# Kernel tuning notes

Hardware: AMD Instinct MI355X
Metric: run time of the kernel (lower is better)

Reference implementation:

```python
import jax, jax.numpy as jnp
import numpy as np

N_TAXA = 32   # N taxa
K = 256       # particles
T = 16        # live subtrees at this step (t = N - r)
R = 16        # merges already done
S = 1024      # alignment sites
A = 4         # DNA alphabet
D = 64        # embedding dim
C = 16        # site-position feature dim
PRIOR_LEN = 0.1


def _expm4(M):
    """Matrix exponential of [..., A, A] via scaling-and-squaring + Taylor."""
    n_sq = 6
    Ms = M / (2.0 ** n_sq)
    I = jnp.eye(M.shape[-1], dtype=M.dtype)
    P = I + Ms
    Tm = Ms
    for i in range(2, 7):
        Tm = jnp.matmul(Tm, Ms) / i
        P = P + Tm
    for _ in range(n_sq):
        P = jnp.matmul(P, P)
    return P


def _stat_probs(emb_ExD, site_SxC, W_stat, W_site):
    # q_matrix_decoder.stat_probs_VxSxA: per-node, per-site stationary probs
    logits = emb_ExD @ W_stat                     # [E, A]
    logits = logits[:, None, :] + site_SxC @ W_site  # [E, S, A]
    return jax.nn.softmax(logits, axis=-1)


def setup_inputs() -> dict:
    key = jax.random.key(0)
    ks = jax.random.split(key, 10)
    ldf = np.zeros(2 * N_TAXA, np.float32)
    for n in range(2, 2 * N_TAXA):
        ldf[n] = ldf[n - 2] + np.log(n)
    return {
        "log_weight_K": jax.random.normal(ks[0], (K,), jnp.float32),
        "branch1_lengths_Kxr": jax.random.uniform(ks[1], (K, R), jnp.float32) * 0.2 + 1e-3,
        "branch2_lengths_Kxr": jax.random.uniform(ks[2], (K, R), jnp.float32) * 0.2 + 1e-3,
        "leaf_counts_Kxt": jnp.ones((K, T), jnp.int32),
        "embeddings_KxtxD": jax.random.normal(ks[3], (K, T, D), jnp.float32),
        "log_felsensteins_KxtxSxA": jax.nn.log_softmax(
            jax.random.normal(ks[4], (K, T, S, A), jnp.float32), axis=-1),
        "log_pi_K": jax.random.normal(ks[5], (K,), jnp.float32),
        "site_positions_SxC": jax.random.uniform(ks[6], (S, C), jnp.float32),
        "W_stat": jax.random.normal(ks[7], (D, A), jnp.float32) * 0.1,
        "W_site": jax.random.normal(ks[8], (C, A), jnp.float32) * 0.1,
        "log_double_factorials_2N": jnp.asarray(ldf),
    }


def reference(log_weight_K, branch1_lengths_Kxr, branch2_lengths_Kxr,
              leaf_counts_Kxt, embeddings_KxtxD, log_felsensteins_KxtxSxA,
              log_pi_K, site_positions_SxC, W_stat, W_site,
              log_double_factorials_2N):
    K_, T_, S_, A_ = log_felsensteins_KxtxSxA.shape
    key = jax.random.key(42)
    kres, ki, koff, ku1, ku2 = jax.random.split(key, 5)

    # ---- SMC categorical resampling over particles ----
    idxK = jax.random.categorical(kres, log_weight_K, shape=(K_,))
    b1r = branch1_lengths_Kxr[idxK]
    b2r = branch2_lengths_Kxr[idxK]
    lc = leaf_counts_Kxt[idxK]
    emb = embeddings_KxtxD[idxK]
    logf = log_felsensteins_KxtxSxA[idxK]
    prev_log_pi = log_pi_K[idxK]

    # ---- proposal (J=1): uniform pair + exponential branch lengths ----
    i = jax.random.randint(ki, (K_,), 0, T_)
    off = jax.random.randint(koff, (K_,), 1, T_)
    j = (i + off) % T_
    idx1 = jnp.minimum(i, j)
    idx2 = jnp.maximum(i, j)
    branch1 = -PRIOR_LEN * jnp.log(jax.random.uniform(ku1, (K_,), minval=1e-6, maxval=1.0))
    branch2 = -PRIOR_LEN * jnp.log(jax.random.uniform(ku2, (K_,), minval=1e-6, maxval=1.0))
    ar = jnp.arange(K_)
    new_emb = 0.5 * (emb[ar, idx1] + emb[ar, idx2])  # [K, D]
    log_v_plus = jnp.log(T_ * (T_ - 1) / 2.0)        # log #pairs

    # ---- merge: put merged value at idx1, move last slot into idx2, drop last ----
    def merge(arr, new_val):
        arr = arr.at[ar, idx1].set(new_val)
        arr = arr.at[ar, idx2].set(arr[ar, T_ - 1])
        return arr[:, :T_ - 1]

    lc_new = merge(lc, lc[ar, idx1] + lc[ar, idx2])   # [K, t-1]
    emb_new = merge(emb, new_emb)                     # [K, t-1, D]

    # ---- Felsenstein pruning step for the merged node ----
    stat = _stat_probs(new_emb, site_positions_SxC, W_stat, W_site)  # [K,S,A]
    Q = jnp.broadcast_to(stat[:, :, None, :], (K_, S_, A_, A_)) - jnp.eye(A_, dtype=stat.dtype)
    P1 = _expm4(Q * branch1[:, None, None, None])  # [K,S,A,A]
    P2 = _expm4(Q * branch2[:, None, None, None])
    f1 = jnp.exp(logf[ar, idx1])  # [K,S,A]
    f2 = jnp.exp(logf[ar, idx2])
    new_logf = (jnp.log(jnp.einsum('ksab,ksb->ksa', P1, f1) + 1e-30)
                + jnp.log(jnp.einsum('ksab,ksb->ksa', P2, f2) + 1e-30))
    logf_new = merge(logf, new_logf)  # [K, t-1, S, A]

    # ---- log pi over the forest: per-subtree likelihood + priors ----
    t_new = T_ - 1
    stat_all = _stat_probs(emb_new.reshape(K_ * t_new, -1), site_positions_SxC,
                           W_stat, W_site).reshape(K_, t_new, S_, A_)
    log_stat = jnp.log(stat_all)
    L = jnp.sum(jax.scipy.special.logsumexp(logf_new + log_stat, axis=-1), axis=-1)  # [K,t-1]
    topo_idx = jnp.clip(2 * lc_new - 3, 0, 2 * N_TAXA - 1)
    topo = -log_double_factorials_2N[topo_idx] * (lc_new >= 2).astype(L.dtype)
    b1_all = jnp.concatenate([b1r, branch1[:, None]], axis=1)  # [K, r+1]
    b2_all = jnp.concatenate([b2r, branch2[:, None]], axis=1)
    prior = (jnp.sum(-b1_all / PRIOR_LEN, axis=1) + jnp.sum(-b2_all / PRIOR_LEN, axis=1)
             - 2.0 * (b1_all.shape[1]) * jnp.log(jnp.asarray(PRIOR_LEN, L.dtype)))
    log_pi_new = jnp.sum(L + topo, axis=1) + prior

    # ---- importance weight ----
    log_v_minus = jnp.log(jnp.maximum(jnp.sum((lc_new > 1).astype(L.dtype), axis=1), 1.0))
    log_weight_new = log_pi_new - prev_log_pi + log_v_minus - log_v_plus
    return log_weight_new
```

## Files before the change

kernel.cpp:

```cpp
#include <hip/hip_runtime.h>
#include <stdint.h>


#define TF_ROT(x0,x1,r) { x0 += x1; x1 = ((x1<<(r))|(x1>>(32-(r)))); x1 ^= x0; }

__host__ __device__ inline void tf2x32(uint32_t k0, uint32_t k1,
                                       uint32_t x0, uint32_t x1,
                                       uint32_t& o0, uint32_t& o1) {
  uint32_t ks2 = k0 ^ k1 ^ 0x1BD11BDAu;
  x0 += k0; x1 += k1;
  TF_ROT(x0,x1,13) TF_ROT(x0,x1,15) TF_ROT(x0,x1,26) TF_ROT(x0,x1,6)
  x0 += k1; x1 += ks2 + 1u;
  TF_ROT(x0,x1,17) TF_ROT(x0,x1,29) TF_ROT(x0,x1,16) TF_ROT(x0,x1,24)
  x0 += ks2; x1 += k0 + 2u;
  TF_ROT(x0,x1,13) TF_ROT(x0,x1,15) TF_ROT(x0,x1,26) TF_ROT(x0,x1,6)
  x0 += k0; x1 += k1 + 3u;
  TF_ROT(x0,x1,17) TF_ROT(x0,x1,29) TF_ROT(x0,x1,16) TF_ROT(x0,x1,24)
  x0 += k1; x1 += ks2 + 4u;
  TF_ROT(x0,x1,13) TF_ROT(x0,x1,15) TF_ROT(x0,x1,26) TF_ROT(x0,x1,6)
  x0 += ks2; x1 += k0 + 5u;
  o0 = x0; o1 = x1;
}

struct Keys {
  uint32_t kres0, kres1;
  uint32_t k2i0, k2i1;
  uint32_t k1o0, k1o1;
  uint32_t k2o0, k2o1;
  uint32_t ku10, ku11;
  uint32_t ku20, ku21;
};

__device__ inline uint32_t rb_fold(uint32_t k0, uint32_t k1, uint32_t i) {
  uint32_t o0, o1;
  tf2x32(k0, k1, 0u, i, o0, o1);
  return o0 ^ o1;
}

__device__ inline float u01f(uint32_t b) {
  return __uint_as_float((b >> 9) | 0x3F800000u) - 1.0f;
}

#define TINYF 1.17549435e-38f

__global__ __launch_bounds__(1024) void k_all(
    const float* __restrict__ logw, const float* __restrict__ b1r,
    const float* __restrict__ b2r, const int* __restrict__ lc,
    const float* __restrict__ emb, const float* __restrict__ lfg,
    const float* __restrict__ logpi, const float* __restrict__ site,
    const float* __restrict__ Wstat, const float* __restrict__ Wsite,
    const float* __restrict__ ldf, float* __restrict__ out, Keys kk) {
  int k = blockIdx.x, tid = threadIdx.x;
  __shared__ float sval[256];
  __shared__ int   sidx[256];
  __shared__ float enl[64];
  __shared__ float sredt[256];
  __shared__ float sredm[16];
  __shared__ float sh_m[4];
  __shared__ float sh_w1, sh_w2, sh_cw;
  __shared__ int   sh_i1, sh_i2;

  if (tid < 256) {
    uint32_t b = rb_fold(kk.kres0, kk.kres1, (uint32_t)(k * 256 + tid));
    float u = fmaxf(TINYF, u01f(b) + TINYF);
    float g = -logf(-logf(u));
    sval[tid] = g + logw[tid];
    sidx[tid] = tid;
  }
  __syncthreads();
  for (int st = 128; st > 0; st >>= 1) {
    if (tid < st) {
      float va = sval[tid], vb = sval[tid + st];
      int ia = sidx[tid], ib = sidx[tid + st];
      if (vb > va || (vb == va && ib < ia)) { sval[tid] = vb; sidx[tid] = ib; }
    }
    __syncthreads();
  }
  int p = sidx[0];

  float es0, es1, es2, es3;
  {
    int s = tid;
    float a0 = 0.f, a1 = 0.f, a2 = 0.f, a3 = 0.f;
#pragma unroll
    for (int c = 0; c < 16; c++) {
      float sc = site[s * 16 + c];
      a0 += sc * Wsite[c * 4 + 0];
      a1 += sc * Wsite[c * 4 + 1];
      a2 += sc * Wsite[c * 4 + 2];
      a3 += sc * Wsite[c * 4 + 3];
    }
    es0 = __expf(a0); es1 = __expf(a1); es2 = __expf(a2); es3 = __expf(a3);
  }

  if (tid >= 64 && tid < 128) {
    int q = tid - 64;
    int t = q >> 2, a = q & 3;
    const float4* e4 = (const float4*)(emb + ((size_t)p * 16 + t) * 64);
    float acc = 0.0f;
#pragma unroll
    for (int d4 = 0; d4 < 16; d4++) {
      float4 e = e4[d4];
      acc += e.x * Wstat[(d4 * 4 + 0) * 4 + a] + e.y * Wstat[(d4 * 4 + 1) * 4 + a] +
             e.z * Wstat[(d4 * 4 + 2) * 4 + a] + e.w * Wstat[(d4 * 4 + 3) * 4 + a];
    }
    enl[q] = __expf(acc);
  }

  if (tid < 5) {
    uint32_t i = rb_fold(kk.k2i0, kk.k2i1, (uint32_t)k) & 15u;
    uint32_t h = rb_fold(kk.k1o0, kk.k1o1, (uint32_t)k) % 15u;
    uint32_t l = rb_fold(kk.k2o0, kk.k2o1, (uint32_t)k) % 15u;
    uint32_t off = 1u + (h + l) % 15u;
    uint32_t j = (i + off) & 15u;
    int i1 = (int)(i < j ? i : j);
    int i2 = (int)(i < j ? j : i);

    if (tid < 4) {
      if (tid == 0) { sh_i1 = i1; sh_i2 = i2; }
      int a = tid;
      const float* e1p = emb + ((size_t)p * 16 + i1) * 64;
      const float* e2p = emb + ((size_t)p * 16 + i2) * 64;
      float acc = 0.0f;
      for (int d = 0; d < 64; d++) acc += 0.5f * (e1p[d] + e2p[d]) * Wstat[d * 4 + a];
      sh_m[a] = __expf(acc);
    } else {
      const float SUBR = 1.0f - 1e-6f;
      float u1 = fmaxf(1e-6f, u01f(rb_fold(kk.ku10, kk.ku11, (uint32_t)k)) * SUBR + 1e-6f);
      float u2 = fmaxf(1e-6f, u01f(rb_fold(kk.ku20, kk.ku21, (uint32_t)k)) * SUBR + 1e-6f);
      float b1 = -0.1f * logf(u1);
      float b2 = -0.1f * logf(u2);
      sh_w1 = 1.0f - expf(-b1);
      sh_w2 = 1.0f - expf(-b2);

      float sb = b1 + b2;
      for (int r = 0; r < 16; r++) sb += b1r[p * 16 + r] + b2r[p * 16 + r];
      float prior = -sb / 0.1f - 34.0f * logf(0.1f);

      float topo_sum = 0.0f; int cnt = 0;
      for (int t = 0; t < 15; t++) {
        int lct;
        if (t == i1)      lct = lc[p * 16 + i1] + lc[p * 16 + i2];
        else if (t == i2) lct = lc[p * 16 + 15];
        else              lct = lc[p * 16 + t];
        int ti = 2 * lct - 3; ti = ti < 0 ? 0 : (ti > 63 ? 63 : ti);
        if (lct >= 2) topo_sum -= ldf[ti];
        if (lct > 1) cnt++;
      }
      float log_v_minus = logf(fmaxf((float)cnt, 1.0f));
      float log_v_plus = logf(120.0f);
      sh_cw = prior + topo_sum - logpi[p] + log_v_minus - log_v_plus;
    }
  }
  __syncthreads();

  const float* base = lfg + (size_t)p * 65536;
  int s = tid;
  float acc[16];
#pragma unroll
  for (int t = 0; t < 16; t++) {
    float4 lf = *(const float4*)(base + t * 4096 + s * 4);
    float w0 = enl[t * 4 + 0] * es0, w1 = enl[t * 4 + 1] * es1;
    float w2 = enl[t * 4 + 2] * es2, w3 = enl[t * 4 + 3] * es3;
    float S1 = w0 + w1 + w2 + w3;
    float S2 = __expf(lf.x) * w0 + __expf(lf.y) * w1 +
               __expf(lf.z) * w2 + __expf(lf.w) * w3;
    acc[t] = __log2f(S2) - __log2f(S1);
  }
#pragma unroll
  for (int t = 0; t < 16; t++) {
    float v = acc[t];
    for (int o = 32; o > 0; o >>= 1) v += __shfl_down(v, o, 64);
    if ((tid & 63) == 0) sredt[t * 16 + (tid >> 6)] = v;
  }

  {
    int i1 = sh_i1, i2 = sh_i2;
    float w1 = sh_w1, w2 = sh_w2;
    float om1 = 1.0f - w1, om2 = 1.0f - w2;
    float m0 = sh_m[0], m1 = sh_m[1], m2 = sh_m[2], m3 = sh_m[3];
    float t0 = m0 * es0, t1 = m1 * es1, t2 = m2 * es2, t3 = m3 * es3;
    float T = t0 + t1 + t2 + t3;
    float invT = 1.0f / T;
    float4 lf1 = *(const float4*)(base + i1 * 4096 + s * 4);
    float4 lf2 = *(const float4*)(base + i2 * 4096 + s * 4);
    float f10 = __expf(lf1.x), f11 = __expf(lf1.y), f12 = __expf(lf1.z), f13 = __expf(lf1.w);
    float f20 = __expf(lf2.x), f21 = __expf(lf2.y), f22 = __expf(lf2.z), f23 = __expf(lf2.w);
    float dot1 = (t0 * f10 + t1 * f11 + t2 * f12 + t3 * f13) * invT;
    float dot2 = (t0 * f20 + t1 * f21 + t2 * f22 + t3 * f23) * invT;
    float n0 = __logf(om1 * f10 + w1 * dot1 + 1e-30f) + __logf(om2 * f20 + w2 * dot2 + 1e-30f);
    float n1 = __logf(om1 * f11 + w1 * dot1 + 1e-30f) + __logf(om2 * f21 + w2 * dot2 + 1e-30f);
    float n2 = __logf(om1 * f12 + w1 * dot1 + 1e-30f) + __logf(om2 * f22 + w2 * dot2 + 1e-30f);
    float n3 = __logf(om1 * f13 + w1 * dot1 + 1e-30f) + __logf(om2 * f23 + w2 * dot2 + 1e-30f);
    float S2 = __expf(n0) * t0 + __expf(n1) * t1 + __expf(n2) * t2 + __expf(n3) * t3;
    float tot = __logf(S2) - __logf(T);

    for (int o = 32; o > 0; o >>= 1) tot += __shfl_down(tot, o, 64);
    if ((tid & 63) == 0) sredm[tid >> 6] = tot;
  }
  __syncthreads();

  if (tid < 64) {
    int t = tid & 15, sb = tid >> 4;
    int i1 = sh_i1, i2 = sh_i2;
    float s4 = sredt[t * 16 + sb * 4 + 0] + sredt[t * 16 + sb * 4 + 1] +
               sredt[t * 16 + sb * 4 + 2] + sredt[t * 16 + sb * 4 + 3];
    float Lv = s4 * 0.69314718056f;
    float coef = (t == i1 || t == i2) ? 0.0f : 1.0f;
    float v = coef * Lv;
    if (tid < 16) v += sredm[tid];
    for (int o = 32; o > 0; o >>= 1) v += __shfl_down(v, o, 64);
    if (tid == 0) out[k] = sh_cw + v;
  }
}

extern "C" void kernel_launch(void* const* d_in, const int* in_sizes, int n_in,
                              void* d_out, int out_size, void* d_ws, size_t ws_size,
                              hipStream_t stream) {
  const float* logw  = (const float*)d_in[0];
  const float* b1r   = (const float*)d_in[1];
  const float* b2r   = (const float*)d_in[2];
  const int*   lc    = (const int*)d_in[3];
  const float* emb   = (const float*)d_in[4];
  const float* lfg   = (const float*)d_in[5];
  const float* logpi = (const float*)d_in[6];
  const float* site  = (const float*)d_in[7];
  const float* Wstat = (const float*)d_in[8];
  const float* Wsite = (const float*)d_in[9];
  const float* ldf   = (const float*)d_in[10];

  uint32_t S0[5], S1[5];
  for (uint32_t i = 0; i < 5; i++) tf2x32(0u, 42u, 0u, i, S0[i], S1[i]);
  Keys kk;
  kk.kres0 = S0[0]; kk.kres1 = S1[0];
  kk.ku10  = S0[3]; kk.ku11  = S1[3];
  kk.ku20  = S0[4]; kk.ku21  = S1[4];
  {
    uint32_t a0, a1, b0, b1;
    tf2x32(S0[1], S1[1], 0u, 0u, a0, a1);
    tf2x32(S0[1], S1[1], 0u, 1u, b0, b1);
    (void)a0; (void)a1;
    kk.k2i0 = b0; kk.k2i1 = b1;
  }
  {
    uint32_t a0, a1, b0, b1;
    tf2x32(S0[2], S1[2], 0u, 0u, a0, a1);
    tf2x32(S0[2], S1[2], 0u, 1u, b0, b1);
    kk.k1o0 = a0; kk.k1o1 = a1;
    kk.k2o0 = b0; kk.k2o1 = b1;
  }

  k_all<<<256, 1024, 0, stream>>>(logw, b1r, b2r, lc, emb, lfg, logpi,
                                  site, Wstat, Wsite, ldf, (float*)d_out, kk);
}
```

Measured before the change: 131.3 us.

## Use wave-shuffle argmax and issue felsenstein loads before the setup sync

The Gumbel-max resampling argmax now uses wavefront shuffles plus a small cross-wave merge, replacing the shared-memory tree with eight barriers. Every thread computes the merge indices itself, and all 16 float4 likelihood loads plus the two merged-subtree loads are issued before the embedding and prior setup barrier, so their memory latency overlaps that work. The site-feature loads become float4, and the launch bounds request more waves per unit. Holding 18 float4 values in registers raises register pressure, which the launch-bounds hint may push toward spills.

After: 133.1 us. Within noise of the previous version (+1.3%).

```diff
diff --git a/kernel.cpp b/kernel.cpp
--- a/kernel.cpp
+++ b/kernel.cpp
@@ -43,7 +43,7 @@
 
 #define TINYF 1.17549435e-38f
 
-__global__ __launch_bounds__(1024) void k_all(
+__global__ __launch_bounds__(1024, 4) void k_all(
     const float* __restrict__ logw, const float* __restrict__ b1r,
     const float* __restrict__ b2r, const int* __restrict__ lc,
     const float* __restrict__ emb, const float* __restrict__ lfg,
@@ -51,47 +51,76 @@
     const float* __restrict__ Wstat, const float* __restrict__ Wsite,
     const float* __restrict__ ldf, float* __restrict__ out, Keys kk) {
   int k = blockIdx.x, tid = threadIdx.x;
-  __shared__ float sval[256];
-  __shared__ int   sidx[256];
+  __shared__ float swv[4];
+  __shared__ int   swi[4];
   __shared__ float enl[64];
   __shared__ float sredt[256];
   __shared__ float sredm[16];
   __shared__ float sh_m[4];
   __shared__ float sh_w1, sh_w2, sh_cw;
-  __shared__ int   sh_i1, sh_i2;
+
+  float es0, es1, es2, es3;
+  {
+    int s = tid;
+    const float4* sp = (const float4*)(site + s * 16);
+    float4 c0 = sp[0], c1 = sp[1], c2 = sp[2], c3 = sp[3];
+    float sc[16] = {c0.x, c0.y, c0.z, c0.w, c1.x, c1.y, c1.z, c1.w,
+                    c2.x, c2.y, c2.z, c2.w, c3.x, c3.y, c3.z, c3.w};
+    float a0 = 0.f, a1 = 0.f, a2 = 0.f, a3 = 0.f;
+#pragma unroll
+    for (int c = 0; c < 16; c++) {
+      a0 += sc[c] * Wsite[c * 4 + 0];
+      a1 += sc[c] * Wsite[c * 4 + 1];
+      a2 += sc[c] * Wsite[c * 4 + 2];
+      a3 += sc[c] * Wsite[c * 4 + 3];
+    }
+    es0 = __expf(a0); es1 = __expf(a1); es2 = __expf(a2); es3 = __expf(a3);
+  }
 
   if (tid < 256) {
     uint32_t b = rb_fold(kk.kres0, kk.kres1, (uint32_t)(k * 256 + tid));
     float u = fmaxf(TINYF, u01f(b) + TINYF);
     float g = -logf(-logf(u));
-    sval[tid] = g + logw[tid];
-    sidx[tid] = tid;
+    float v = g + logw[tid];
+    int idx = tid;
+    for (int o = 32; o > 0; o >>= 1) {
+      float vo = __shfl_down(v, o, 64);
+      int   io = __shfl_down(idx, o, 64);
+      if (vo > v || (vo == v && io < idx)) { v = vo; idx = io; }
+    }
+    if ((tid & 63) == 0) { swv[tid >> 6] = v; swi[tid >> 6] = idx; }
   }
   __syncthreads();
-  for (int st = 128; st > 0; st >>= 1) {
-    if (tid < st) {
-      float va = sval[tid], vb = sval[tid + st];
-      int ia = sidx[tid], ib = sidx[tid + st];
-      if (vb > va || (vb == va && ib < ia)) { sval[tid] = vb; sidx[tid] = ib; }
-    }
-    __syncthreads();
-  }
-  int p = sidx[0];
-
-  float es0, es1, es2, es3;
-  {
-    int s = tid;
-    float a0 = 0.f, a1 = 0.f, a2 = 0.f, a3 = 0.f;
-#pragma unroll
-    for (int c = 0; c < 16; c++) {
-      float sc = site[s * 16 + c];
-      a0 += sc * Wsite[c * 4 + 0];
-      a1 += sc * Wsite[c * 4 + 1];
-      a2 += sc * Wsite[c * 4 + 2];
-      a3 += sc * Wsite[c * 4 + 3];
-    }
-    es0 = __expf(a0); es1 = __expf(a1); es2 = __expf(a2); es3 = __expf(a3);
-  }
+  int p;
+  {
+    float bv = swv[0]; int bi = swi[0];
+#pragma unroll
+    for (int w = 1; w < 4; w++) {
+      float vo = swv[w]; int io = swi[w];
+      if (vo > bv || (vo == bv && io < bi)) { bv = vo; bi = io; }
+    }
+    p = bi;
+  }
+
+  int i1, i2;
+  {
+    uint32_t i = rb_fold(kk.k2i0, kk.k2i1, (uint32_t)k) & 15u;
+    uint32_t h = rb_fold(kk.k1o0, kk.k1o1, (uint32_t)k) % 15u;
+    uint32_t l = rb_fold(kk.k2o0, kk.k2o1, (uint32_t)k) % 15u;
+    uint32_t off = 1u + (h + l) % 15u;
+    uint32_t j = (i + off) & 15u;
+    i1 = (int)(i < j ? i : j);
+    i2 = (int)(i < j ? j : i);
+  }
+
+  const float* base = lfg + (size_t)p * 65536;
+  int s = tid;
+  float4 lfv[16];
+#pragma unroll
+  for (int t = 0; t < 16; t++)
+    lfv[t] = *(const float4*)(base + t * 4096 + s * 4);
+  float4 lf1 = *(const float4*)(base + i1 * 4096 + s * 4);
+  float4 lf2 = *(const float4*)(base + i2 * 4096 + s * 4);
 
   if (tid >= 64 && tid < 128) {
     int q = tid - 64;
@@ -107,83 +136,67 @@
     enl[q] = __expf(acc);
   }
 
-  if (tid < 5) {
-    uint32_t i = rb_fold(kk.k2i0, kk.k2i1, (uint32_t)k) & 15u;
-    uint32_t h = rb_fold(kk.k1o0, kk.k1o1, (uint32_t)k) % 15u;
-    uint32_t l = rb_fold(kk.k2o0, kk.k2o1, (uint32_t)k) % 15u;
-    uint32_t off = 1u + (h + l) % 15u;
-    uint32_t j = (i + off) & 15u;
-    int i1 = (int)(i < j ? i : j);
-    int i2 = (int)(i < j ? j : i);
-
-    if (tid < 4) {
-      if (tid == 0) { sh_i1 = i1; sh_i2 = i2; }
-      int a = tid;
-      const float* e1p = emb + ((size_t)p * 16 + i1) * 64;
-      const float* e2p = emb + ((size_t)p * 16 + i2) * 64;
-      float acc = 0.0f;
-      for (int d = 0; d < 64; d++) acc += 0.5f * (e1p[d] + e2p[d]) * Wstat[d * 4 + a];
-      sh_m[a] = __expf(acc);
-    } else {
-      const float SUBR = 1.0f - 1e-6f;
-      float u1 = fmaxf(1e-6f, u01f(rb_fold(kk.ku10, kk.ku11, (uint32_t)k)) * SUBR + 1e-6f);
-      float u2 = fmaxf(1e-6f, u01f(rb_fold(kk.ku20, kk.ku21, (uint32_t)k)) * SUBR + 1e-6f);
-      float b1 = -0.1f * logf(u1);
-      float b2 = -0.1f * logf(u2);
-      sh_w1 = 1.0f - expf(-b1);
-      sh_w2 = 1.0f - expf(-b2);
-
-      float sb = b1 + b2;
-      for (int r = 0; r < 16; r++) sb += b1r[p * 16 + r] + b2r[p * 16 + r];
-      float prior = -sb / 0.1f - 34.0f * logf(0.1f);
-
-      float topo_sum = 0.0f; int cnt = 0;
-      for (int t = 0; t < 15; t++) {
-        int lct;
-        if (t == i1)      lct = lc[p * 16 + i1] + lc[p * 16 + i2];
-        else if (t == i2) lct = lc[p * 16 + 15];
-        else              lct = lc[p * 16 + t];
-        int ti = 2 * lct - 3; ti = ti < 0 ? 0 : (ti > 63 ? 63 : ti);
-        if (lct >= 2) topo_sum -= ldf[ti];
-        if (lct > 1) cnt++;
-      }
-      float log_v_minus = logf(fmaxf((float)cnt, 1.0f));
-      float log_v_plus = logf(120.0f);
-      sh_cw = prior + topo_sum - logpi[p] + log_v_minus - log_v_plus;
-    }
+  if (tid < 4) {
+    int a = tid;
+    const float* e1p = emb + ((size_t)p * 16 + i1) * 64;
+    const float* e2p = emb + ((size_t)p * 16 + i2) * 64;
+    float acc = 0.0f;
+    for (int d = 0; d < 64; d++) acc += 0.5f * (e1p[d] + e2p[d]) * Wstat[d * 4 + a];
+    sh_m[a] = __expf(acc);
+  } else if (tid == 4) {
+    const float SUBR = 1.0f - 1e-6f;
+    float u1 = fmaxf(1e-6f, u01f(rb_fold(kk.ku10, kk.ku11, (uint32_t)k)) * SUBR + 1e-6f);
+    float u2 = fmaxf(1e-6f, u01f(rb_fold(kk.ku20, kk.ku21, (uint32_t)k)) * SUBR + 1e-6f);
+    float b1 = -0.1f * logf(u1);
+    float b2 = -0.1f * logf(u2);
+    sh_w1 = 1.0f - expf(-b1);
+    sh_w2 = 1.0f - expf(-b2);
+
+    float sb = b1 + b2;
+    for (int r = 0; r < 16; r++) sb += b1r[p * 16 + r] + b2r[p * 16 + r];
+    float prior = -sb / 0.1f - 34.0f * logf(0.1f);
+
+    float topo_sum = 0.0f; int cnt = 0;
+    for (int t = 0; t < 15; t++) {
+      int lct;
+      if (t == i1)      lct = lc[p * 16 + i1] + lc[p * 16 + i2];
+      else if (t == i2) lct = lc[p * 16 + 15];
+      else              lct = lc[p * 16 + t];
+      int ti = 2 * lct - 3; ti = ti < 0 ? 0 : (ti > 63 ? 63 : ti);
+      if (lct >= 2) topo_sum -= ldf[ti];
+      if (lct > 1) cnt++;
+    }
+    float log_v_minus = logf(fmaxf((float)cnt, 1.0f));
+    float log_v_plus = logf(120.0f);
+    sh_cw = prior + topo_sum - logpi[p] + log_v_minus - log_v_plus;
   }
   __syncthreads();
 
-  const float* base = lfg + (size_t)p * 65536;
-  int s = tid;
-  float acc[16];
+  float accv[16];
 #pragma unroll
   for (int t = 0; t < 16; t++) {
-    float4 lf = *(const float4*)(base + t * 4096 + s * 4);
+    float4 lf = lfv[t];
     float w0 = enl[t * 4 + 0] * es0, w1 = enl[t * 4 + 1] * es1;
     float w2 = enl[t * 4 + 2] * es2, w3 = enl[t * 4 + 3] * es3;
     float S1 = w0 + w1 + w2 + w3;
     float S2 = __expf(lf.x) * w0 + __expf(lf.y) * w1 +
                __expf(lf.z) * w2 + __expf(lf.w) * w3;
-    acc[t] = __log2f(S2) - __log2f(S1);
+    accv[t] = __log2f(S2) - __log2f(S1);
   }
 #pragma unroll
   for (int t = 0; t < 16; t++) {
-    float v = acc[t];
+    float v = accv[t];
     for (int o = 32; o > 0; o >>= 1) v += __shfl_down(v, o, 64);
     if ((tid & 63) == 0) sredt[t * 16 + (tid >> 6)] = v;
   }
 
   {
-    int i1 = sh_i1, i2 = sh_i2;
     float w1 = sh_w1, w2 = sh_w2;
     float om1 = 1.0f - w1, om2 = 1.0f - w2;
     float m0 = sh_m[0], m1 = sh_m[1], m2 = sh_m[2], m3 = sh_m[3];
     float t0 = m0 * es0, t1 = m1 * es1, t2 = m2 * es2, t3 = m3 * es3;
     float T = t0 + t1 + t2 + t3;
     float invT = 1.0f / T;
-    float4 lf1 = *(const float4*)(base + i1 * 4096 + s * 4);
-    float4 lf2 = *(const float4*)(base + i2 * 4096 + s * 4);
     float f10 = __expf(lf1.x), f11 = __expf(lf1.y), f12 = __expf(lf1.z), f13 = __expf(lf1.w);
     float f20 = __expf(lf2.x), f21 = __expf(lf2.y), f22 = __expf(lf2.z), f23 = __expf(lf2.w);
     float dot1 = (t0 * f10 + t1 * f11 + t2 * f12 + t3 * f13) * invT;
@@ -202,7 +215,6 @@
 
   if (tid < 64) {
     int t = tid & 15, sb = tid >> 4;
-    int i1 = sh_i1, i2 = sh_i2;
     float s4 = sredt[t * 16 + sb * 4 + 0] + sredt[t * 16 + sb * 4 + 1] +
                sredt[t * 16 + sb * 4 + 2] + sredt[t * 16 + sb * 4 + 3];
     float Lv = s4 * 0.69314718056f;
```
